# Performance work log

Measured on AMD Instinct MI355X. Metric: run time of the kernel, lower is better.

Reference implementation:

```python
import jax, jax.numpy as jnp
import numpy as np

EMBED_DIM = 32
DELTA_V = 0.5
DELTA_D = 3.0
NUM_LABELS = 20  # instance labels are 1..NUM_LABELS; 0 is background


def _safe_sqrt(x):
    # sqrt with zero-safe gradient (matches norm of identical points -> 0)
    s = jnp.where(x > 0, x, 1.0)
    return jnp.where(x > 0, jnp.sqrt(s), 0.0)


def _per_batch(emb, seg):
    # emb: [D, N], seg: [N] int labels in 0..L (0 = background)
    D, N = emb.shape
    L = NUM_LABELS
    dt = emb.dtype
    ones = jnp.ones((N,), dt)
    counts = jax.ops.segment_sum(ones, seg, num_segments=L + 1)          # [L+1]
    sums = jax.ops.segment_sum(emb.T, seg, num_segments=L + 1)          # [L+1, D]
    means = sums / jnp.maximum(counts, 1.0)[:, None]                     # [L+1, D]
    present = (counts > 0).at[0].set(False)                              # [L+1]
    num_lanes = jnp.sum(present.astype(dt))

    # --- variance (pull) loss: each pixel vs its own instance centroid ---
    mpix = means[seg]                                                    # [N, D] gather
    sq = jnp.sum((emb.T - mpix) ** 2, axis=1)                            # [N]
    d = _safe_sqrt(sq)
    v = jnp.maximum(d - DELTA_V, 0.0) ** 2 * (seg > 0).astype(dt)        # background excluded
    vsum = jax.ops.segment_sum(v, seg, num_segments=L + 1)               # [L+1]
    vmean = vsum / jnp.maximum(counts, 1.0)
    var_loss = jnp.sum(vmean * present.astype(dt)) / jnp.maximum(num_lanes, 1.0)
    var_loss = jnp.where(num_lanes > 0, var_loss, jnp.zeros((), dt))

    # --- distance (push) loss between present centroids ---
    m = means[1:]                                                        # [L, D]
    p = present[1:]                                                      # [L]
    sqd = jnp.sum((m[:, None, :] - m[None, :, :]) ** 2, axis=-1)         # [L, L]
    dist = _safe_sqrt(sqd)
    pair = (p[:, None] & p[None, :]) & ~jnp.eye(L, dtype=bool)
    dl = jnp.sum(jnp.maximum(DELTA_D - dist, 0.0) ** 2 * pair.astype(dt))
    denom = jnp.maximum(num_lanes * (num_lanes - 1.0), 1.0)
    dist_loss = jnp.where(num_lanes > 1, dl / denom / 2.0, jnp.zeros((), dt))
    return var_loss, dist_loss


def setup_inputs() -> dict:
    key = jax.random.key(0)
    k1, k2 = jax.random.split(key)
    B, D, N = 8, EMBED_DIM, 65536  # 256x256 BEV raster flattened
    embedding = jax.random.normal(k1, (B, D, N), dtype=jnp.float32)
    seg_gt = jax.random.randint(k2, (B, N), 0, NUM_LABELS + 1, dtype=jnp.int32)
    return {"embedding": embedding, "seg_gt": seg_gt}


def reference(embedding, seg_gt):
    var_b, dist_b = jax.vmap(_per_batch)(embedding, seg_gt)  # [B], [B]
    var_loss = jnp.mean(var_b)
    dist_loss = jnp.mean(dist_b)
    reg_loss = jnp.zeros((), embedding.dtype)
    return (var_loss, dist_loss, reg_loss)
```

## Files before the change

### kernel.cpp

```cpp
#include <hip/hip_runtime.h>
#include <hip/hip_cooperative_groups.h>
namespace cg = cooperative_groups;

#define NSEG 21
#define NLBL 20
#define DIM  32
#define NS   64
#define NREP 16
#define DV   0.5f
#define DD   3.0f
#define BATCH 8
#define N_PIX 65536
#define SMS  36
#define DYNB (128*512 + 1024)

using short8 = __attribute__((ext_vector_type(8))) short;
using f32x4  = __attribute__((ext_vector_type(4))) float;

#define P_OFF  0
#define C2_OFF (BATCH*DIM*NLBL*NS)
#define M_OFF  (C2_OFF + BATCH*NLBL*NS)
#define CN_OFF (M_OFF + BATCH*NLBL*DIM)
#define V_OFF  (CN_OFF + BATCH*NLBL)
#define PB_OFF (V_OFF + BATCH*NLBL*NS)

__device__ __forceinline__ short bf16rne(float f) {
  const unsigned u = __builtin_bit_cast(unsigned, f);
  return (short)((u + 0x7FFFu + ((u >> 16) & 1u)) >> 16);
}

__device__ __forceinline__ void momentsBody(const float* __restrict__ emb,
                                            const int* __restrict__ seg,
                                            float* __restrict__ ws,
                                            float* lred, ushort* tile,
                                            unsigned char* segt,
                                            int bx, int b, int tid) {
  const int wv = tid >> 6, lane = tid & 63;
  const int lr = lane & 15, lg = lane >> 4;
  const float* rowA0 = emb + ((size_t)b * DIM + lr) * N_PIX;
  const float* rowA1 = rowA0 + (size_t)16 * N_PIX;
  const int*   segb  = seg + (size_t)b * N_PIX;

  f32x4 s00 = {0,0,0,0}, s01 = {0,0,0,0}, s10 = {0,0,0,0}, s11 = {0,0,0,0};
  f32x4 c0  = {0,0,0,0}, c1  = {0,0,0,0};
  short8 ones;
  #pragma unroll
  for (int j = 0; j < 8; ++j) ones[j] = (short)0x3F80;

  #pragma unroll 2
  for (int t = 0; t < 8; ++t) {
    const int kl = wv * 256 + t * 32 + lg * 8;
    const int koff = bx * 1024 + kl;
    const float4 a00 = *(const float4*)(rowA0 + koff);
    const float4 a01 = *(const float4*)(rowA0 + koff + 4);
    const float4 a10 = *(const float4*)(rowA1 + koff);
    const float4 a11 = *(const float4*)(rowA1 + koff + 4);
    const int4   g0  = *(const int4*)(segb + koff);
    const int4   g1  = *(const int4*)(segb + koff + 4);

    short8 fa0, fa1, fb0, fb1;
    fa0[0] = bf16rne(a00.x); fa0[1] = bf16rne(a00.y);
    fa0[2] = bf16rne(a00.z); fa0[3] = bf16rne(a00.w);
    fa0[4] = bf16rne(a01.x); fa0[5] = bf16rne(a01.y);
    fa0[6] = bf16rne(a01.z); fa0[7] = bf16rne(a01.w);
    fa1[0] = bf16rne(a10.x); fa1[1] = bf16rne(a10.y);
    fa1[2] = bf16rne(a10.z); fa1[3] = bf16rne(a10.w);
    fa1[4] = bf16rne(a11.x); fa1[5] = bf16rne(a11.y);
    fa1[6] = bf16rne(a11.z); fa1[7] = bf16rne(a11.w);
    const int lab0 = lr + 1, lab1 = lr + 17;
    fb0[0] = (g0.x == lab0) ? (short)0x3F80 : (short)0;
    fb0[1] = (g0.y == lab0) ? (short)0x3F80 : (short)0;
    fb0[2] = (g0.z == lab0) ? (short)0x3F80 : (short)0;
    fb0[3] = (g0.w == lab0) ? (short)0x3F80 : (short)0;
    fb0[4] = (g1.x == lab0) ? (short)0x3F80 : (short)0;
    fb0[5] = (g1.y == lab0) ? (short)0x3F80 : (short)0;
    fb0[6] = (g1.z == lab0) ? (short)0x3F80 : (short)0;
    fb0[7] = (g1.w == lab0) ? (short)0x3F80 : (short)0;
    fb1[0] = (g0.x == lab1) ? (short)0x3F80 : (short)0;
    fb1[1] = (g0.y == lab1) ? (short)0x3F80 : (short)0;
    fb1[2] = (g0.z == lab1) ? (short)0x3F80 : (short)0;
    fb1[3] = (g0.w == lab1) ? (short)0x3F80 : (short)0;
    fb1[4] = (g1.x == lab1) ? (short)0x3F80 : (short)0;
    fb1[5] = (g1.y == lab1) ? (short)0x3F80 : (short)0;
    fb1[6] = (g1.z == lab1) ? (short)0x3F80 : (short)0;
    fb1[7] = (g1.w == lab1) ? (short)0x3F80 : (short)0;

    const int o = kl >> 3, om = o & 7;
    *(short8*)&tile[o * 256 + ((lr ^ om) << 3)] = fa0;
    *(short8*)&tile[o * 256 + (((lr ^ om) + 16) << 3)] = fa1;
    if (lr == 0) {
      unsigned long long pk =
          (unsigned long long)(g0.x & 255)        | ((unsigned long long)(g0.y & 255) << 8) |
          ((unsigned long long)(g0.z & 255) << 16) | ((unsigned long long)(g0.w & 255) << 24) |
          ((unsigned long long)(g1.x & 255) << 32) | ((unsigned long long)(g1.y & 255) << 40) |
          ((unsigned long long)(g1.z & 255) << 48) | ((unsigned long long)(g1.w & 255) << 56);
      *(unsigned long long*)&segt[o * 8] = pk;
    }

    s00 = __builtin_amdgcn_mfma_f32_16x16x32_bf16(fa0, fb0, s00, 0, 0, 0);
    s01 = __builtin_amdgcn_mfma_f32_16x16x32_bf16(fa0, fb1, s01, 0, 0, 0);
    s10 = __builtin_amdgcn_mfma_f32_16x16x32_bf16(fa1, fb0, s10, 0, 0, 0);
    s11 = __builtin_amdgcn_mfma_f32_16x16x32_bf16(fa1, fb1, s11, 0, 0, 0);
    c0  = __builtin_amdgcn_mfma_f32_16x16x32_bf16(ones, fb0, c0, 0, 0, 0);
    c1  = __builtin_amdgcn_mfma_f32_16x16x32_bf16(ones, fb1, c1, 0, 0, 0);
  }

  float vals[24];
  #pragma unroll
  for (int r = 0; r < 4; ++r) {
    vals[0 * 4 + r] = s00[r]; vals[1 * 4 + r] = s01[r];
    vals[2 * 4 + r] = s10[r]; vals[3 * 4 + r] = s11[r];
    vals[4 * 4 + r] = c0[r];  vals[5 * 4 + r] = c1[r];
  }
  #pragma unroll
  for (int w = 0; w < 4; ++w) {
    if (wv == w) {
      float* base = lred + lane * 4;
      if (w == 0) {
        #pragma unroll
        for (int f = 0; f < 6; ++f)
          #pragma unroll
          for (int r = 0; r < 4; ++r) base[f * 256 + r] = vals[f * 4 + r];
      } else {
        #pragma unroll
        for (int f = 0; f < 6; ++f)
          #pragma unroll
          for (int r = 0; r < 4; ++r) base[f * 256 + r] += vals[f * 4 + r];
      }
    }
    __syncthreads();
  }
  for (int i = tid; i < 1536; i += 256) {
    const float v = lred[i];
    const int f = i >> 8, ln = (i >> 2) & 63, r = i & 3;
    const int col = ln & 15, row = ((ln >> 4) << 2) | r;
    if (f < 4) {
      const int d = (f >> 1) * 16 + row;
      const int lcol = (f & 1) * 16 + col;
      if (lcol < NLBL)
        ws[P_OFF + (((size_t)(b * DIM + d) * NLBL) + lcol) * NS + bx] = v;
    } else {
      const int lcol = (f & 1) * 16 + col;
      if (row == 0 && lcol < NLBL)
        ws[C2_OFF + ((size_t)b * NLBL + lcol) * NS + bx] = v;
    }
  }
}

__device__ __forceinline__ void meansBody(float* __restrict__ ws, float* s_c,
                                          int bx8, int b, int tid) {
  if (tid < NLBL) {
    const float4* cp = (const float4*)(ws + C2_OFF + ((size_t)b * NLBL + tid) * NS);
    float q0 = 0.f, q1 = 0.f, q2 = 0.f, q3 = 0.f;
    #pragma unroll
    for (int k = 0; k < NS / 4; k += 4) {
      const float4 v0 = cp[k], v1 = cp[k + 1], v2 = cp[k + 2], v3 = cp[k + 3];
      q0 += v0.x + v0.y + v0.z + v0.w;
      q1 += v1.x + v1.y + v1.z + v1.w;
      q2 += v2.x + v2.y + v2.z + v2.w;
      q3 += v3.x + v3.y + v3.z + v3.w;
    }
    const float c = q0 + q1 + q2 + q3;
    if (bx8 == 0) ws[CN_OFF + b * NLBL + tid] = c;
    s_c[tid] = fmaxf(c, 1.f);
  }
  __syncthreads();
  if (tid < 80) {
    const int m = bx8 * 80 + tid;
    const int l = m >> 5, d = m & 31;
    const float4* pp = (const float4*)(ws + P_OFF + (((size_t)(b * DIM + d) * NLBL) + l) * NS);
    float q0 = 0.f, q1 = 0.f, q2 = 0.f, q3 = 0.f;
    #pragma unroll
    for (int k = 0; k < NS / 4; k += 4) {
      const float4 v0 = pp[k], v1 = pp[k + 1], v2 = pp[k + 2], v3 = pp[k + 3];
      q0 += v0.x + v0.y + v0.z + v0.w;
      q1 += v1.x + v1.y + v1.z + v1.w;
      q2 += v2.x + v2.y + v2.z + v2.w;
      q3 += v3.x + v3.y + v3.z + v3.w;
    }
    ws[M_OFF + (size_t)b * NLBL * DIM + m] = (q0 + q1 + q2 + q3) / s_c[l];
  }
}

__device__ __forceinline__ void loadMeans(const float* __restrict__ ws,
                                          float* s_m, int b, int tid) {
  for (int i = tid; i < NSEG * SMS; i += 256) s_m[i] = 0.f;
  __syncthreads();
  if (tid < 160) {
    const float4 v = ((const float4*)(ws + M_OFF + (size_t)b * NLBL * DIM))[tid];
    const int flat = tid * 4, l = flat >> 5, d = flat & 31;
    float* dst = &s_m[(l + 1) * SMS + d];
    dst[0] = v.x; dst[1] = v.y; dst[2] = v.z; dst[3] = v.w;
  }
}

__device__ __forceinline__ void finalBody(float* __restrict__ ws,
                                          float* s_m, float* s_c, float* s_vs,
                                          int* s_p, float* s_red, int b, int tid) {
  const int wv = tid >> 6, lane = tid & 63;
  if (tid < 160) {
    const int g = tid >> 3, j = tid & 7;
    const float4* v4 = (const float4*)(ws + V_OFF + ((size_t)b * NLBL + g) * NS + j * 8);
    const float4 a = v4[0], c = v4[1];
    float s = a.x + a.y + a.z + a.w + c.x + c.y + c.z + c.w;
    s += __shfl_xor(s, 1, 64); s += __shfl_xor(s, 2, 64); s += __shfl_xor(s, 4, 64);
    if (j == 0) s_vs[g] = s;
  }
  if (tid < NLBL) {
    const float c = ws[CN_OFF + b * NLBL + tid];
    s_c[tid] = c;
    s_p[tid] = (c > 0.f) ? 1 : 0;
  }
  __syncthreads();
  loadMeans(ws, s_m, b, tid);
  __syncthreads();

  float dl = 0.f;
  for (int p = tid; p < NLBL * NLBL; p += 256) {
    const int i = p / NLBL, j = p - (p / NLBL) * NLBL;
    if (i != j && s_p[i] && s_p[j]) {
      float sq = 0.f;
      #pragma unroll
      for (int d = 0; d < DIM; ++d) {
        const float t = s_m[(i + 1) * SMS + d] - s_m[(j + 1) * SMS + d];
        sq += t * t;
      }
      const float r = DD - sqrtf(sq);
      if (r > 0.f) dl += r * r;
    }
  }
  #pragma unroll
  for (int off = 32; off; off >>= 1) dl += __shfl_xor(dl, off, 64);
  if (lane == 0) s_red[wv] = dl;
  __syncthreads();
  if (tid == 0) {
    const float dsum = s_red[0] + s_red[1] + s_red[2] + s_red[3];
    float nl = 0.f, var = 0.f;
    for (int l = 0; l < NLBL; ++l)
      if (s_p[l]) { nl += 1.f; var += s_vs[l] / s_c[l]; }
    ws[PB_OFF + b * 2]     = (nl > 0.f) ? var / nl : 0.f;
    ws[PB_OFF + b * 2 + 1] = (nl > 1.f) ? dsum / fmaxf(nl * (nl - 1.f), 1.f) * 0.5f : 0.f;
  }
}

__device__ __forceinline__ void outBody(const float* __restrict__ ws,
                                        float* __restrict__ out, int tid) {
  if (tid < 64) {
    float v = 0.f, d = 0.f;
    if (tid < BATCH) {
      v = ws[PB_OFF + tid * 2];
      d = ws[PB_OFF + tid * 2 + 1];
    }
    #pragma unroll
    for (int off = 4; off; off >>= 1) { v += __shfl_xor(v, off, 64); d += __shfl_xor(d, off, 64); }
    if (tid == 0) {
      out[0] = v / (float)BATCH;
      out[1] = d / (float)BATCH;
      out[2] = 0.f;
    }
  }
}

__global__ __launch_bounds__(256, 2)
void k_fused(const float* __restrict__ emb, const int* __restrict__ seg,
             float* __restrict__ ws, float* __restrict__ out) {
  extern __shared__ __align__(16) char dynls[];
  ushort* tile = (ushort*)dynls;
  unsigned char* segt = (unsigned char*)(dynls + 65536);
  __shared__ __align__(16) float lred[1536];
  __shared__ __align__(16) float s_m[NSEG * SMS];
  __shared__ float s_v[NREP * NSEG];
  __shared__ float s_c[NLBL];
  __shared__ float s_vs[NLBL];
  __shared__ int   s_p[NLBL];
  __shared__ float s_red[4];
  cg::grid_group gg = cg::this_grid();
  const int tid = threadIdx.x, bx = blockIdx.x, b = blockIdx.y;

  momentsBody(emb, seg, ws, lred, tile, segt, bx, b, tid);
  gg.sync();
  if (bx < 8) meansBody(ws, s_c, bx, b, tid);
  gg.sync();

  for (int i = tid; i < NREP * NSEG; i += 256) s_v[i] = 0.f;
  loadMeans(ws, s_m, b, tid);
  __syncthreads();
  {
    const int px0 = tid * 4;
    const int o = px0 >> 3, om = o & 7, p8 = px0 & 7;
    const int la0 = segt[px0], la1 = segt[px0 + 1], la2 = segt[px0 + 2], la3 = segt[px0 + 3];
    float q0 = 0.f, q1 = 0.f, q2 = 0.f, q3 = 0.f;
    #pragma unroll
    for (int db = 0; db < 8; ++db) {
      const f32x4 m0 = *(const f32x4*)&s_m[la0 * SMS + db * 4];
      const f32x4 m1 = *(const f32x4*)&s_m[la1 * SMS + db * 4];
      const f32x4 m2 = *(const f32x4*)&s_m[la2 * SMS + db * 4];
      const f32x4 m3 = *(const f32x4*)&s_m[la3 * SMS + db * 4];
      #pragma unroll
      for (int dd = 0; dd < 4; ++dd) {
        const int d = db * 4 + dd;
        const ushort4 ev = *(const ushort4*)&tile[o * 256 + ((d ^ om) << 3) + p8];
        float t;
        t = __builtin_bit_cast(float, (unsigned)ev.x << 16) - m0[dd]; q0 += t * t;
        t = __builtin_bit_cast(float, (unsigned)ev.y << 16) - m1[dd]; q1 += t * t;
        t = __builtin_bit_cast(float, (unsigned)ev.z << 16) - m2[dd]; q2 += t * t;
        t = __builtin_bit_cast(float, (unsigned)ev.w << 16) - m3[dd]; q3 += t * t;
      }
    }
    const int rb = (tid & (NREP - 1)) * NSEG;
    if (la0 > 0) { const float r = sqrtf(q0) - DV; if (r > 0.f) atomicAdd(&s_v[rb + la0], r * r); }
    if (la1 > 0) { const float r = sqrtf(q1) - DV; if (r > 0.f) atomicAdd(&s_v[rb + la1], r * r); }
    if (la2 > 0) { const float r = sqrtf(q2) - DV; if (r > 0.f) atomicAdd(&s_v[rb + la2], r * r); }
    if (la3 > 0) { const float r = sqrtf(q3) - DV; if (r > 0.f) atomicAdd(&s_v[rb + la3], r * r); }
  }
  __syncthreads();
  if (tid < NLBL) {
    float v = 0.f;
    #pragma unroll
    for (int r = 0; r < NREP; ++r) v += s_v[r * NSEG + (tid + 1)];
    ws[V_OFF + ((size_t)b * NLBL + tid) * NS + bx] = v;
  }
  gg.sync();
  if (bx == 0) finalBody(ws, s_m, s_c, s_vs, s_p, s_red, b, tid);
  gg.sync();
  if (bx == 0 && b == 0) outBody(ws, out, tid);
}

__global__ __launch_bounds__(256)
void k_moments(const float* __restrict__ emb, const int* __restrict__ seg,
               float* __restrict__ ws) {
  extern __shared__ __align__(16) char dynls[];
  ushort* tile = (ushort*)dynls;
  unsigned char* segt = (unsigned char*)(dynls + 65536);
  __shared__ __align__(16) float lred[1536];
  momentsBody(emb, seg, ws, lred, tile, segt, blockIdx.x, blockIdx.y, threadIdx.x);
}
__global__ __launch_bounds__(256)
void k_means(float* __restrict__ ws) {
  __shared__ float s_c[NLBL];
  meansBody(ws, s_c, blockIdx.x, blockIdx.y, threadIdx.x);
}
__global__ __launch_bounds__(256)
void k_varG(const float* __restrict__ emb, const int* __restrict__ seg,
            float* __restrict__ ws) {
  __shared__ __align__(16) float s_m[NSEG * SMS];
  __shared__ float s_v[NREP * NSEG];
  const int tid = threadIdx.x, bx = blockIdx.x, b = blockIdx.y;
  for (int i = tid; i < NREP * NSEG; i += 256) s_v[i] = 0.f;
  loadMeans(ws, s_m, b, tid);
  __syncthreads();
  const int n0 = bx * 1024 + tid * 4;
  const int4 sl = *(const int4*)(seg + (size_t)b * N_PIX + n0);
  const float4* e4 = (const float4*)(emb + (size_t)b * DIM * N_PIX + n0);
  float q0 = 0.f, q1 = 0.f, q2 = 0.f, q3 = 0.f;
  #pragma unroll 8
  for (int d = 0; d < DIM; ++d) {
    const float4 e = e4[d * (N_PIX / 4)];
    float t;
    t = e.x - s_m[sl.x * SMS + d]; q0 += t * t;
    t = e.y - s_m[sl.y * SMS + d]; q1 += t * t;
    t = e.z - s_m[sl.z * SMS + d]; q2 += t * t;
    t = e.w - s_m[sl.w * SMS + d]; q3 += t * t;
  }
  const int rb = (tid & (NREP - 1)) * NSEG;
  if (sl.x > 0) { const float r = sqrtf(q0) - DV; if (r > 0.f) atomicAdd(&s_v[rb + sl.x], r * r); }
  if (sl.y > 0) { const float r = sqrtf(q1) - DV; if (r > 0.f) atomicAdd(&s_v[rb + sl.y], r * r); }
  if (sl.z > 0) { const float r = sqrtf(q2) - DV; if (r > 0.f) atomicAdd(&s_v[rb + sl.z], r * r); }
  if (sl.w > 0) { const float r = sqrtf(q3) - DV; if (r > 0.f) atomicAdd(&s_v[rb + sl.w], r * r); }
  __syncthreads();
  if (tid < NLBL) {
    float v = 0.f;
    #pragma unroll
    for (int r = 0; r < NREP; ++r) v += s_v[r * NSEG + (tid + 1)];
    ws[V_OFF + ((size_t)b * NLBL + tid) * NS + bx] = v;
  }
}
__global__ __launch_bounds__(256)
void k_final(float* __restrict__ ws) {
  __shared__ __align__(16) float s_m[NSEG * SMS];
  __shared__ float s_c[NLBL];
  __shared__ float s_vs[NLBL];
  __shared__ int   s_p[NLBL];
  __shared__ float s_red[4];
  finalBody(ws, s_m, s_c, s_vs, s_p, s_red, blockIdx.x, threadIdx.x);
}
__global__ __launch_bounds__(64)
void k_out(const float* __restrict__ ws, float* __restrict__ out) {
  outBody(ws, out, threadIdx.x);
}

extern "C" void kernel_launch(void* const* d_in, const int* in_sizes, int n_in,
                              void* d_out, int out_size, void* d_ws, size_t ws_size,
                              hipStream_t stream) {
  const float* emb = (const float*)d_in[0];
  const int*   seg = (const int*)d_in[1];
  float* out = (float*)d_out;
  float* ws  = (float*)d_ws;

  int maxB = 0;
  bool coop = false;
  if (hipOccupancyMaxActiveBlocksPerMultiprocessor(&maxB, (const void*)k_fused, 256, DYNB)
        == hipSuccess)
    coop = ((long)maxB * 256 >= (long)NS * BATCH);
  if (coop) {
    void* args[] = {(void*)&emb, (void*)&seg, (void*)&ws, (void*)&out};
    if (hipLaunchCooperativeKernel((const void*)k_fused, dim3(NS, BATCH), dim3(256),
                                   args, DYNB, stream) == hipSuccess)
      return;
  }
  k_moments<<<dim3(NS, BATCH), 256, DYNB, stream>>>(emb, seg, ws);
  k_means  <<<dim3(8, BATCH), 256, 0, stream>>>(ws);
  k_varG   <<<dim3(NS, BATCH), 256, 0, stream>>>(emb, seg, ws);
  k_final  <<<dim3(BATCH), 256, 0, stream>>>(ws);
  k_out    <<<1, 64, 0, stream>>>(ws, out);
}
```

Before: 43.19 us.

## Replace final grid syncs with per-batch last-block atomic reduction

Drops the last two grid-wide barriers of the cooperative kernel. Each block now atomically accumulates its per-label variance sums into a small workspace area and bumps a per-batch arrival counter, and the last block to arrive for a batch computes that batch's losses and atomically adds them into the output. This needs two extra memset launches before the kernel to zero the counters, accumulators and output. The float atomics make the summation order nondeterministic.

```diff
diff --git a/kernel.cpp b/kernel.cpp
--- a/kernel.cpp
+++ b/kernel.cpp
@@ -12,7 +12,9 @@
 #define BATCH 8
 #define N_PIX 65536
 #define SMS  36
-#define DYNB (128*512 + 1024)
+#define TILE_B 65536
+#define SEGT_B 1024
+#define DYNB  (TILE_B + SEGT_B)
 
 using short8 = __attribute__((ext_vector_type(8))) short;
 using f32x4  = __attribute__((ext_vector_type(4))) float;
@@ -21,7 +23,9 @@
 #define C2_OFF (BATCH*DIM*NLBL*NS)
 #define M_OFF  (C2_OFF + BATCH*NLBL*NS)
 #define CN_OFF (M_OFF + BATCH*NLBL*DIM)
-#define V_OFF  (CN_OFF + BATCH*NLBL)
+#define VS_OFF (CN_OFF + BATCH*NLBL)
+#define BAR_OFF (VS_OFF + 8*BATCH*NLBL)
+#define V_OFF  (BAR_OFF + 8)
 #define PB_OFF (V_OFF + BATCH*NLBL*NS)
 
 __device__ __forceinline__ short bf16rne(float f) {
@@ -194,10 +198,186 @@
   }
 }
 
-__device__ __forceinline__ void finalBody(float* __restrict__ ws,
-                                          float* s_m, float* s_c, float* s_vs,
-                                          int* s_p, float* s_red, int b, int tid) {
+__device__ __forceinline__ void varTileCompute(const ushort* tile,
+                                               const unsigned char* segt,
+                                               const float* s_m, float* s_v,
+                                               int tid) {
+  const int px0 = tid * 4;
+  const int o = px0 >> 3, om = o & 7, p8 = px0 & 7;
+  const int la0 = segt[px0], la1 = segt[px0 + 1], la2 = segt[px0 + 2], la3 = segt[px0 + 3];
+  float q0 = 0.f, q1 = 0.f, q2 = 0.f, q3 = 0.f;
+  #pragma unroll
+  for (int db = 0; db < 8; ++db) {
+    const f32x4 m0 = *(const f32x4*)&s_m[la0 * SMS + db * 4];
+    const f32x4 m1 = *(const f32x4*)&s_m[la1 * SMS + db * 4];
+    const f32x4 m2 = *(const f32x4*)&s_m[la2 * SMS + db * 4];
+    const f32x4 m3 = *(const f32x4*)&s_m[la3 * SMS + db * 4];
+    #pragma unroll
+    for (int dd = 0; dd < 4; ++dd) {
+      const int d = db * 4 + dd;
+      const ushort4 ev = *(const ushort4*)&tile[o * 256 + ((d ^ om) << 3) + p8];
+      float t;
+      t = __builtin_bit_cast(float, (unsigned)ev.x << 16) - m0[dd]; q0 += t * t;
+      t = __builtin_bit_cast(float, (unsigned)ev.y << 16) - m1[dd]; q1 += t * t;
+      t = __builtin_bit_cast(float, (unsigned)ev.z << 16) - m2[dd]; q2 += t * t;
+      t = __builtin_bit_cast(float, (unsigned)ev.w << 16) - m3[dd]; q3 += t * t;
+    }
+  }
+  const int rb = (tid & (NREP - 1)) * NSEG;
+  if (la0 > 0) { const float r = sqrtf(q0) - DV; if (r > 0.f) atomicAdd(&s_v[rb + la0], r * r); }
+  if (la1 > 0) { const float r = sqrtf(q1) - DV; if (r > 0.f) atomicAdd(&s_v[rb + la1], r * r); }
+  if (la2 > 0) { const float r = sqrtf(q2) - DV; if (r > 0.f) atomicAdd(&s_v[rb + la2], r * r); }
+  if (la3 > 0) { const float r = sqrtf(q3) - DV; if (r > 0.f) atomicAdd(&s_v[rb + la3], r * r); }
+}
+
+__global__ __launch_bounds__(256, 2)
+void k_fused(const float* __restrict__ emb, const int* __restrict__ seg,
+             float* __restrict__ ws, float* __restrict__ out) {
+  extern __shared__ __align__(16) char dynls[];
+  ushort* tile = (ushort*)dynls;
+  unsigned char* segt = (unsigned char*)(dynls + TILE_B);
+  __shared__ __align__(16) float lred[1536];
+  __shared__ __align__(16) float s_m[NSEG * SMS];
+  __shared__ float s_v[NREP * NSEG];
+  __shared__ float s_c[NLBL];
+  __shared__ float s_vs[NLBL];
+  __shared__ int   s_p[NLBL];
+  __shared__ float s_red[4];
+  __shared__ int   s_last;
+  cg::grid_group gg = cg::this_grid();
+  const int tid = threadIdx.x, bx = blockIdx.x, b = blockIdx.y;
   const int wv = tid >> 6, lane = tid & 63;
+
+  momentsBody(emb, seg, ws, lred, tile, segt, bx, b, tid);
+  gg.sync();
+
+  if (bx < 8) meansBody(ws, s_c, bx, b, tid);
+  gg.sync();
+
+  for (int i = tid; i < NREP * NSEG; i += 256) s_v[i] = 0.f;
+  loadMeans(ws, s_m, b, tid);
+  __syncthreads();
+  varTileCompute(tile, segt, s_m, s_v, tid);
+  __syncthreads();
+  if (tid < NLBL) {
+    float v = 0.f;
+    #pragma unroll
+    for (int r = 0; r < NREP; ++r) v += s_v[r * NSEG + (tid + 1)];
+    atomicAdd(&ws[VS_OFF + ((size_t)(bx & 7) * BATCH + b) * NLBL + tid], v);
+  }
+  __syncthreads();
+  if (tid == 0) {
+    __threadfence();
+    unsigned* ctr = (unsigned*)(ws + BAR_OFF);
+    s_last = (atomicAdd(&ctr[b], 1u) == NS - 1) ? 1 : 0;
+  }
+  __syncthreads();
+
+  if (s_last) {
+    __threadfence();
+    if (tid < 160) {
+      const int g = tid >> 3, j = tid & 7;
+      float s = atomicAdd(&ws[VS_OFF + ((size_t)j * BATCH + b) * NLBL + g], 0.f);
+      s += __shfl_xor(s, 1, 64); s += __shfl_xor(s, 2, 64); s += __shfl_xor(s, 4, 64);
+      if (j == 0) s_vs[g] = s;
+    }
+    if (tid < NLBL) {
+      const float c = ws[CN_OFF + b * NLBL + tid];
+      s_c[tid] = c;
+      s_p[tid] = (c > 0.f) ? 1 : 0;
+    }
+    __syncthreads();
+    float dl = 0.f;
+    for (int p = tid; p < NLBL * NLBL; p += 256) {
+      const int i = p / NLBL, j = p - (p / NLBL) * NLBL;
+      if (i != j && s_p[i] && s_p[j]) {
+        float sq = 0.f;
+        #pragma unroll
+        for (int d = 0; d < DIM; ++d) {
+          const float t = s_m[(i + 1) * SMS + d] - s_m[(j + 1) * SMS + d];
+          sq += t * t;
+        }
+        const float r = DD - sqrtf(sq);
+        if (r > 0.f) dl += r * r;
+      }
+    }
+    #pragma unroll
+    for (int off = 32; off; off >>= 1) dl += __shfl_xor(dl, off, 64);
+    if (lane == 0) s_red[wv] = dl;
+    __syncthreads();
+    if (tid == 0) {
+      const float dsum = s_red[0] + s_red[1] + s_red[2] + s_red[3];
+      float nl = 0.f, var = 0.f;
+      for (int l = 0; l < NLBL; ++l)
+        if (s_p[l]) { nl += 1.f; var += s_vs[l] / s_c[l]; }
+      const float vb  = (nl > 0.f) ? var / nl : 0.f;
+      const float db_ = (nl > 1.f) ? dsum / fmaxf(nl * (nl - 1.f), 1.f) * 0.5f : 0.f;
+      atomicAdd(&out[0], vb * (1.f / BATCH));
+      atomicAdd(&out[1], db_ * (1.f / BATCH));
+    }
+  }
+}
+
+__global__ __launch_bounds__(256)
+void k_moments(const float* __restrict__ emb, const int* __restrict__ seg,
+               float* __restrict__ ws) {
+  extern __shared__ __align__(16) char dynls[];
+  ushort* tile = (ushort*)dynls;
+  unsigned char* segt = (unsigned char*)(dynls + TILE_B);
+  __shared__ __align__(16) float lred[1536];
+  momentsBody(emb, seg, ws, lred, tile, segt, blockIdx.x, blockIdx.y, threadIdx.x);
+}
+__global__ __launch_bounds__(256)
+void k_means(float* __restrict__ ws) {
+  __shared__ float s_c[NLBL];
+  meansBody(ws, s_c, blockIdx.x, blockIdx.y, threadIdx.x);
+}
+__global__ __launch_bounds__(256)
+void k_varG(const float* __restrict__ emb, const int* __restrict__ seg,
+            float* __restrict__ ws) {
+  __shared__ __align__(16) float s_m[NSEG * SMS];
+  __shared__ float s_v[NREP * NSEG];
+  const int tid = threadIdx.x, bx = blockIdx.x, b = blockIdx.y;
+  for (int i = tid; i < NREP * NSEG; i += 256) s_v[i] = 0.f;
+  loadMeans(ws, s_m, b, tid);
+  __syncthreads();
+  const int n0 = bx * 1024 + tid * 4;
+  const int4 sl = *(const int4*)(seg + (size_t)b * N_PIX + n0);
+  const float4* e4 = (const float4*)(emb + (size_t)b * DIM * N_PIX + n0);
+  float q0 = 0.f, q1 = 0.f, q2 = 0.f, q3 = 0.f;
+  #pragma unroll 8
+  for (int d = 0; d < DIM; ++d) {
+    const float4 e = e4[d * (N_PIX / 4)];
+    float t;
+    t = e.x - s_m[sl.x * SMS + d]; q0 += t * t;
+    t = e.y - s_m[sl.y * SMS + d]; q1 += t * t;
+    t = e.z - s_m[sl.z * SMS + d]; q2 += t * t;
+    t = e.w - s_m[sl.w * SMS + d]; q3 += t * t;
+  }
+  const int rb = (tid & (NREP - 1)) * NSEG;
+  if (sl.x > 0) { const float r = sqrtf(q0) - DV; if (r > 0.f) atomicAdd(&s_v[rb + sl.x], r * r); }
+  if (sl.y > 0) { const float r = sqrtf(q1) - DV; if (r > 0.f) atomicAdd(&s_v[rb + sl.y], r * r); }
+  if (sl.z > 0) { const float r = sqrtf(q2) - DV; if (r > 0.f) atomicAdd(&s_v[rb + sl.z], r * r); }
+  if (sl.w > 0) { const float r = sqrtf(q3) - DV; if (r > 0.f) atomicAdd(&s_v[rb + sl.w], r * r); }
+  __syncthreads();
+  if (tid < NLBL) {
+    float v = 0.f;
+    #pragma unroll
+    for (int r = 0; r < NREP; ++r) v += s_v[r * NSEG + (tid + 1)];
+    ws[V_OFF + ((size_t)b * NLBL + tid) * NS + bx] = v;
+  }
+}
+__global__ __launch_bounds__(256)
+void k_final(float* __restrict__ ws) {
+  __shared__ __align__(16) float s_m[NSEG * SMS];
+  __shared__ float s_c[NLBL];
+  __shared__ float s_vs[NLBL];
+  __shared__ int   s_p[NLBL];
+  __shared__ float s_red[4];
+  const int b = blockIdx.x, tid = threadIdx.x;
+  const int wv = tid >> 6, lane = tid & 63;
+  loadMeans(ws, s_m, b, tid);
+  __syncthreads();
   if (tid < 160) {
     const int g = tid >> 3, j = tid & 7;
     const float4* v4 = (const float4*)(ws + V_OFF + ((size_t)b * NLBL + g) * NS + j * 8);
@@ -212,9 +392,6 @@
     s_p[tid] = (c > 0.f) ? 1 : 0;
   }
   __syncthreads();
-  loadMeans(ws, s_m, b, tid);
-  __syncthreads();
-
   float dl = 0.f;
   for (int p = tid; p < NLBL * NLBL; p += 256) {
     const int i = p / NLBL, j = p - (p / NLBL) * NLBL;
@@ -242,151 +419,21 @@
     ws[PB_OFF + b * 2 + 1] = (nl > 1.f) ? dsum / fmaxf(nl * (nl - 1.f), 1.f) * 0.5f : 0.f;
   }
 }
-
-__device__ __forceinline__ void outBody(const float* __restrict__ ws,
-                                        float* __restrict__ out, int tid) {
-  if (tid < 64) {
-    float v = 0.f, d = 0.f;
-    if (tid < BATCH) {
-      v = ws[PB_OFF + tid * 2];
-      d = ws[PB_OFF + tid * 2 + 1];
-    }
-    #pragma unroll
-    for (int off = 4; off; off >>= 1) { v += __shfl_xor(v, off, 64); d += __shfl_xor(d, off, 64); }
-    if (tid == 0) {
-      out[0] = v / (float)BATCH;
-      out[1] = d / (float)BATCH;
-      out[2] = 0.f;
-    }
-  }
-}
-
-__global__ __launch_bounds__(256, 2)
-void k_fused(const float* __restrict__ emb, const int* __restrict__ seg,
-             float* __restrict__ ws, float* __restrict__ out) {
-  extern __shared__ __align__(16) char dynls[];
-  ushort* tile = (ushort*)dynls;
-  unsigned char* segt = (unsigned char*)(dynls + 65536);
-  __shared__ __align__(16) float lred[1536];
-  __shared__ __align__(16) float s_m[NSEG * SMS];
-  __shared__ float s_v[NREP * NSEG];
-  __shared__ float s_c[NLBL];
-  __shared__ float s_vs[NLBL];
-  __shared__ int   s_p[NLBL];
-  __shared__ float s_red[4];
-  cg::grid_group gg = cg::this_grid();
-  const int tid = threadIdx.x, bx = blockIdx.x, b = blockIdx.y;
-
-  momentsBody(emb, seg, ws, lred, tile, segt, bx, b, tid);
-  gg.sync();
-  if (bx < 8) meansBody(ws, s_c, bx, b, tid);
-  gg.sync();
-
-  for (int i = tid; i < NREP * NSEG; i += 256) s_v[i] = 0.f;
-  loadMeans(ws, s_m, b, tid);
-  __syncthreads();
-  {
-    const int px0 = tid * 4;
-    const int o = px0 >> 3, om = o & 7, p8 = px0 & 7;
-    const int la0 = segt[px0], la1 = segt[px0 + 1], la2 = segt[px0 + 2], la3 = segt[px0 + 3];
-    float q0 = 0.f, q1 = 0.f, q2 = 0.f, q3 = 0.f;
-    #pragma unroll
-    for (int db = 0; db < 8; ++db) {
-      const f32x4 m0 = *(const f32x4*)&s_m[la0 * SMS + db * 4];
-      const f32x4 m1 = *(const f32x4*)&s_m[la1 * SMS + db * 4];
-      const f32x4 m2 = *(const f32x4*)&s_m[la2 * SMS + db * 4];
-      const f32x4 m3 = *(const f32x4*)&s_m[la3 * SMS + db * 4];
-      #pragma unroll
-      for (int dd = 0; dd < 4; ++dd) {
-        const int d = db * 4 + dd;
-        const ushort4 ev = *(const ushort4*)&tile[o * 256 + ((d ^ om) << 3) + p8];
-        float t;
-        t = __builtin_bit_cast(float, (unsigned)ev.x << 16) - m0[dd]; q0 += t * t;
-        t = __builtin_bit_cast(float, (unsigned)ev.y << 16) - m1[dd]; q1 += t * t;
-        t = __builtin_bit_cast(float, (unsigned)ev.z << 16) - m2[dd]; q2 += t * t;
-        t = __builtin_bit_cast(float, (unsigned)ev.w << 16) - m3[dd]; q3 += t * t;
-      }
-    }
-    const int rb = (tid & (NREP - 1)) * NSEG;
-    if (la0 > 0) { const float r = sqrtf(q0) - DV; if (r > 0.f) atomicAdd(&s_v[rb + la0], r * r); }
-    if (la1 > 0) { const float r = sqrtf(q1) - DV; if (r > 0.f) atomicAdd(&s_v[rb + la1], r * r); }
-    if (la2 > 0) { const float r = sqrtf(q2) - DV; if (r > 0.f) atomicAdd(&s_v[rb + la2], r * r); }
-    if (la3 > 0) { const float r = sqrtf(q3) - DV; if (r > 0.f) atomicAdd(&s_v[rb + la3], r * r); }
-  }
-  __syncthreads();
-  if (tid < NLBL) {
-    float v = 0.f;
-    #pragma unroll
-    for (int r = 0; r < NREP; ++r) v += s_v[r * NSEG + (tid + 1)];
-    ws[V_OFF + ((size_t)b * NLBL + tid) * NS + bx] = v;
-  }
-  gg.sync();
-  if (bx == 0) finalBody(ws, s_m, s_c, s_vs, s_p, s_red, b, tid);
-  gg.sync();
-  if (bx == 0 && b == 0) outBody(ws, out, tid);
-}
-
-__global__ __launch_bounds__(256)
-void k_moments(const float* __restrict__ emb, const int* __restrict__ seg,
-               float* __restrict__ ws) {
-  extern __shared__ __align__(16) char dynls[];
-  ushort* tile = (ushort*)dynls;
-  unsigned char* segt = (unsigned char*)(dynls + 65536);
-  __shared__ __align__(16) float lred[1536];
-  momentsBody(emb, seg, ws, lred, tile, segt, blockIdx.x, blockIdx.y, threadIdx.x);
-}
-__global__ __launch_bounds__(256)
-void k_means(float* __restrict__ ws) {
-  __shared__ float s_c[NLBL];
-  meansBody(ws, s_c, blockIdx.x, blockIdx.y, threadIdx.x);
-}
-__global__ __launch_bounds__(256)
-void k_varG(const float* __restrict__ emb, const int* __restrict__ seg,
-            float* __restrict__ ws) {
-  __shared__ __align__(16) float s_m[NSEG * SMS];
-  __shared__ float s_v[NREP * NSEG];
-  const int tid = threadIdx.x, bx = blockIdx.x, b = blockIdx.y;
-  for (int i = tid; i < NREP * NSEG; i += 256) s_v[i] = 0.f;
-  loadMeans(ws, s_m, b, tid);
-  __syncthreads();
-  const int n0 = bx * 1024 + tid * 4;
-  const int4 sl = *(const int4*)(seg + (size_t)b * N_PIX + n0);
-  const float4* e4 = (const float4*)(emb + (size_t)b * DIM * N_PIX + n0);
-  float q0 = 0.f, q1 = 0.f, q2 = 0.f, q3 = 0.f;
-  #pragma unroll 8
-  for (int d = 0; d < DIM; ++d) {
-    const float4 e = e4[d * (N_PIX / 4)];
-    float t;
-    t = e.x - s_m[sl.x * SMS + d]; q0 += t * t;
-    t = e.y - s_m[sl.y * SMS + d]; q1 += t * t;
-    t = e.z - s_m[sl.z * SMS + d]; q2 += t * t;
-    t = e.w - s_m[sl.w * SMS + d]; q3 += t * t;
-  }
-  const int rb = (tid & (NREP - 1)) * NSEG;
-  if (sl.x > 0) { const float r = sqrtf(q0) - DV; if (r > 0.f) atomicAdd(&s_v[rb + sl.x], r * r); }
-  if (sl.y > 0) { const float r = sqrtf(q1) - DV; if (r > 0.f) atomicAdd(&s_v[rb + sl.y], r * r); }
-  if (sl.z > 0) { const float r = sqrtf(q2) - DV; if (r > 0.f) atomicAdd(&s_v[rb + sl.z], r * r); }
-  if (sl.w > 0) { const float r = sqrtf(q3) - DV; if (r > 0.f) atomicAdd(&s_v[rb + sl.w], r * r); }
-  __syncthreads();
-  if (tid < NLBL) {
-    float v = 0.f;
-    #pragma unroll
-    for (int r = 0; r < NREP; ++r) v += s_v[r * NSEG + (tid + 1)];
-    ws[V_OFF + ((size_t)b * NLBL + tid) * NS + bx] = v;
-  }
-}
-__global__ __launch_bounds__(256)
-void k_final(float* __restrict__ ws) {
-  __shared__ __align__(16) float s_m[NSEG * SMS];
-  __shared__ float s_c[NLBL];
-  __shared__ float s_vs[NLBL];
-  __shared__ int   s_p[NLBL];
-  __shared__ float s_red[4];
-  finalBody(ws, s_m, s_c, s_vs, s_p, s_red, blockIdx.x, threadIdx.x);
-}
 __global__ __launch_bounds__(64)
 void k_out(const float* __restrict__ ws, float* __restrict__ out) {
-  outBody(ws, out, threadIdx.x);
+  const int tid = threadIdx.x;
+  float v = 0.f, d = 0.f;
+  if (tid < BATCH) {
+    v = ws[PB_OFF + tid * 2];
+    d = ws[PB_OFF + tid * 2 + 1];
+  }
+  #pragma unroll
+  for (int off = 4; off; off >>= 1) { v += __shfl_xor(v, off, 64); d += __shfl_xor(d, off, 64); }
+  if (tid == 0) {
+    out[0] = v / (float)BATCH;
+    out[1] = d / (float)BATCH;
+    out[2] = 0.f;
+  }
 }
 
 extern "C" void kernel_launch(void* const* d_in, const int* in_sizes, int n_in,
@@ -403,6 +450,8 @@
         == hipSuccess)
     coop = ((long)maxB * 256 >= (long)NS * BATCH);
   if (coop) {
+    hipMemsetAsync(ws + VS_OFF, 0, (8 * BATCH * NLBL + 8) * sizeof(float), stream);
+    hipMemsetAsync(d_out, 0, (size_t)out_size * sizeof(float), stream);
     void* args[] = {(void*)&emb, (void*)&seg, (void*)&ws, (void*)&out};
     if (hipLaunchCooperativeKernel((const void*)k_fused, dim3(NS, BATCH), dim3(256),
                                    args, DYNB, stream) == hipSuccess)
```

After: 42.84 us. No clear change (-0.8%).
